# Kernel tuning notes

Hardware: AMD Instinct MI355X
Metric: run time of the kernel (lower is better)

Reference implementation:

```python
import jax, jax.numpy as jnp
from jax import lax
import numpy as np

STRIDE = 1
PADDING = 1
THRESHOLD = 0.25
DECAY = 0.9


def setup_inputs() -> dict:
    key = jax.random.key(0)
    k1, k2 = jax.random.split(key)
    B, Cin, L, T = 16, 32, 1024, 64
    Cout, K = 64, 3
    x = jax.random.uniform(k1, (B, Cin, L, T), dtype=jnp.float32)
    weight = jax.random.normal(k2, (Cout, Cin, K), dtype=jnp.float32) * 0.1
    return {"x": x, "weight": weight}


def reference(x, weight):
    # x: (B, Cin, L, T); weight: (Cout, Cin, K)
    B, Cin, L, T = x.shape
    Cout, _, K = weight.shape
    # Conv1d applied to every timestep at once: fold T into the batch dim.
    xt = jnp.transpose(x, (0, 3, 1, 2)).reshape(B * T, Cin, L)  # (B*T, Cin, L)
    act = lax.conv_general_dilated(
        xt, weight,
        window_strides=(STRIDE,),
        padding=[(PADDING, PADDING)],
        dimension_numbers=("NCH", "OIH", "NCH"),
    )  # (B*T, Cout, OL)
    OL = act.shape[-1]
    act = act.reshape(B, T, Cout, OL).transpose(1, 0, 2, 3)  # (T, B, Cout, OL)

    def step(pot, a):
        # LIF update: integrate, decay, threshold, reset (matches original order).
        pot = (pot + a) * DECAY
        spk = (pot >= THRESHOLD).astype(pot.dtype)
        pot = jnp.where(spk > 0, jnp.zeros_like(pot), pot)
        return pot, spk

    pot0 = jnp.zeros((B, Cout, OL), dtype=x.dtype)
    _, spikes = lax.scan(step, pot0, act)  # spikes: (T, B, Cout, OL)
    return jnp.transpose(spikes, (1, 2, 3, 0))  # (B, Cout, OL, T)
```

## Files before the change

### kernel.cpp

```cpp
#include <hip/hip_runtime.h>
#include <math.h>

#define BB    16
#define CIN   32
#define LEN   1024
#define TT    64
#define COUT  64
#define KK    3

#define TL      32
#define HALO    (TL + 2)
#define TCH     8
#define PADT    12
#define CO_PER  8
#define NTHREADS 256
#define NROWS   (CIN * HALO)
#define NITEM   (NROWS * 2)
#define NPRE    ((NITEM + NTHREADS - 1) / NTHREADS)


__device__ __forceinline__ float4 load_item(const float* __restrict__ xb,
                                            int l0, int tc, int idx) {
    const int row = idx >> 1;
    const int h   = idx & 1;
    const int ci  = row / HALO;
    const int ll  = row % HALO;
    const int lg  = l0 - 1 + ll;
    float4 v = make_float4(0.f, 0.f, 0.f, 0.f);
    if (lg >= 0 && lg < LEN)
        v = *(const float4*)(xb + ((size_t)ci * LEN + lg) * TT + tc * TCH + h * 4);
    return v;
}

__global__ __launch_bounds__(NTHREADS)
void snn_v3(const float* __restrict__ x, const float* __restrict__ w,
            float* __restrict__ out) {
    __shared__ float xs[CIN][HALO][PADT];

    const int tid  = threadIdx.x;
    const int l    = tid & 31;
    const int half = (tid >> 5) & 1;
    const int wvu  = __builtin_amdgcn_readfirstlane(tid >> 6);
    const int coA  = wvu * 16;
    const int l0   = blockIdx.x * TL;
    const int b    = blockIdx.y;

    const float* xb   = x   + (size_t)b * CIN * LEN * TT;
    float*       outb = out + (size_t)b * COUT * LEN * TT;

    float pot[CO_PER];
    #pragma unroll
    for (int j = 0; j < CO_PER; ++j) pot[j] = 0.0f;

    float4 pre[NPRE];
    {
        int i = 0;
        for (int idx = tid; idx < NITEM; idx += NTHREADS, ++i)
            pre[i] = load_item(xb, l0, 0, idx);
    }

    for (int tc = 0; tc < TT / TCH; ++tc) {
        __syncthreads();
        {
            int i = 0;
            for (int idx = tid; idx < NITEM; idx += NTHREADS, ++i) {
                const int row = idx >> 1;
                const int h   = idx & 1;
                *(float4*)&xs[row / HALO][row % HALO][h * 4] = pre[i];
            }
        }
        __syncthreads();
        if (tc + 1 < TT / TCH) {
            int i = 0;
            for (int idx = tid; idx < NITEM; idx += NTHREADS, ++i)
                pre[i] = load_item(xb, l0, tc + 1, idx);
        }

        float acc[CO_PER][TCH];
        #pragma unroll
        for (int j = 0; j < CO_PER; ++j)
            #pragma unroll
            for (int i = 0; i < TCH; ++i) acc[j][i] = 0.0f;

        #pragma unroll
        for (int k = 0; k < KK; ++k) {
            for (int ci = 0; ci < CIN; ++ci) {
                const float4 xa = *(const float4*)&xs[ci][l + k][0];
                const float4 xc = *(const float4*)&xs[ci][l + k][4];
                #pragma unroll
                for (int j = 0; j < CO_PER; ++j) {
                    const float wA = w[((coA + j)     * CIN + ci) * KK + k];
                    const float wB = w[((coA + 8 + j) * CIN + ci) * KK + k];
                    const float wj = half ? wB : wA;
                    acc[j][0] = fmaf(xa.x, wj, acc[j][0]);
                    acc[j][1] = fmaf(xa.y, wj, acc[j][1]);
                    acc[j][2] = fmaf(xa.z, wj, acc[j][2]);
                    acc[j][3] = fmaf(xa.w, wj, acc[j][3]);
                    acc[j][4] = fmaf(xc.x, wj, acc[j][4]);
                    acc[j][5] = fmaf(xc.y, wj, acc[j][5]);
                    acc[j][6] = fmaf(xc.z, wj, acc[j][6]);
                    acc[j][7] = fmaf(xc.w, wj, acc[j][7]);
                }
            }
        }

        const int co0 = coA + half * 8;
        #pragma unroll
        for (int j = 0; j < CO_PER; ++j) {
            float sv[TCH];
            #pragma unroll
            for (int i = 0; i < TCH; ++i) {
                const float s = pot[j] + acc[j][i];
                const float p = s * 0.9f;
                const bool spk = (p >= 0.25f);
                sv[i]  = spk ? 1.0f : 0.0f;
                pot[j] = spk ? 0.0f : p;
            }
            float* dst = outb + ((size_t)(co0 + j) * LEN + (l0 + l)) * TT
                              + tc * TCH;
            *(float4*)(dst)     = make_float4(sv[0], sv[1], sv[2], sv[3]);
            *(float4*)(dst + 4) = make_float4(sv[4], sv[5], sv[6], sv[7]);
        }
    }
}

extern "C" void kernel_launch(void* const* d_in, const int* in_sizes, int n_in,
                              void* d_out, int out_size, void* d_ws, size_t ws_size,
                              hipStream_t stream) {
    const float* x = (const float*)d_in[0];
    const float* w = (const float*)d_in[1];
    float* out = (float*)d_out;
    (void)d_ws; (void)ws_size; (void)in_sizes; (void)n_in; (void)out_size;

    hipLaunchKernelGGL(snn_v3, dim3(LEN / TL, BB), dim3(NTHREADS),
                       0, stream, x, w, out);
}
```

Baseline: 722.6 us.

## Restructure SNN conv kernel with smaller tiles, swizzled LDS and bit-packed spikes

Shrinks the L tile to 16 positions and gives each thread 4 output channels instead of 8. The time axis is staged in 16-wide chunks through an XOR-swizzled float4 shared buffer. Spikes are collected into bitmasks in registers and written once at the end as contiguous 64-float rows per output channel, replacing the strided per-chunk writes. The aim is higher occupancy (launch bounds 4), fewer LDS bank conflicts and more coalesced stores. In exchange the grid has twice as many blocks with more halo reloads, and the software prefetch across chunks is gone.

```diff
diff --git a/kernel.cpp b/kernel.cpp
--- a/kernel.cpp
+++ b/kernel.cpp
@@ -1,5 +1,4 @@
 #include <hip/hip_runtime.h>
-#include <math.h>
 
 #define BB    16
 #define CIN   32
@@ -8,118 +7,140 @@
 #define COUT  64
 #define KK    3
 
-#define TL      32
-#define HALO    (TL + 2)
-#define TCH     8
-#define PADT    12
-#define CO_PER  8
+#define TL       16
+#define HALO     (TL + 2)
 #define NTHREADS 256
-#define NROWS   (CIN * HALO)
-#define NITEM   (NROWS * 2)
-#define NPRE    ((NITEM + NTHREADS - 1) / NTHREADS)
+#define CO_PER   4
+#define NGRAN    (CIN * HALO * 4)
+#define NRND     (NGRAN / 64)
+#define SPT      (NRND / 4)
 
 
-__device__ __forceinline__ float4 load_item(const float* __restrict__ xb,
-                                            int l0, int tc, int idx) {
-    const int row = idx >> 1;
-    const int h   = idx & 1;
-    const int ci  = row / HALO;
-    const int ll  = row % HALO;
-    const int lg  = l0 - 1 + ll;
-    float4 v = make_float4(0.f, 0.f, 0.f, 0.f);
-    if (lg >= 0 && lg < LEN)
-        v = *(const float4*)(xb + ((size_t)ci * LEN + lg) * TT + tc * TCH + h * 4);
-    return v;
-}
-
-__global__ __launch_bounds__(NTHREADS)
-void snn_v3(const float* __restrict__ x, const float* __restrict__ w,
+__global__ __launch_bounds__(NTHREADS, 4)
+void snn_v4(const float* __restrict__ x, const float* __restrict__ w,
             float* __restrict__ out) {
-    __shared__ float xs[CIN][HALO][PADT];
+    __shared__ float4 xs[NGRAN];
 
     const int tid  = threadIdx.x;
-    const int l    = tid & 31;
-    const int half = (tid >> 5) & 1;
-    const int wvu  = __builtin_amdgcn_readfirstlane(tid >> 6);
-    const int coA  = wvu * 16;
+    const int l    = tid & (TL - 1);
+    const int g    = tid >> 4;
+    const int co0  = g * CO_PER;
+    const int lane = tid & 63;
+    const int wv   = tid >> 6;
     const int l0   = blockIdx.x * TL;
     const int b    = blockIdx.y;
 
-    const float* xb   = x   + (size_t)b * CIN * LEN * TT;
-    float*       outb = out + (size_t)b * COUT * LEN * TT;
+    const float* xb = x + (size_t)b * CIN * LEN * TT;
+    const float* wb = w + co0 * (CIN * KK);
 
-    float pot[CO_PER];
+    int goff[SPT], loff[SPT];
+    unsigned okb = 0u;
     #pragma unroll
-    for (int j = 0; j < CO_PER; ++j) pot[j] = 0.0f;
-
-    float4 pre[NPRE];
-    {
-        int i = 0;
-        for (int idx = tid; idx < NITEM; idx += NTHREADS, ++i)
-            pre[i] = load_item(xb, l0, 0, idx);
+    for (int s = 0; s < SPT; ++s) {
+        const int G   = (wv + s * 4) * 64 + lane;
+        const int ci  = G / (HALO * 4);
+        const int rem = G - ci * (HALO * 4);
+        const int row = rem >> 2;
+        const int h   = rem & 3;
+        const int lg  = l0 - 1 + row;
+        const bool ok = (lg >= 0) && (lg < LEN);
+        okb |= ok ? (1u << s) : 0u;
+        goff[s] = (ci * LEN + (ok ? lg : 0)) * TT + h * 4;
+        loff[s] = ci * (HALO * 4) + row * 4 + (h ^ ((row >> 1) & 3));
     }
 
-    for (int tc = 0; tc < TT / TCH; ++tc) {
-        __syncthreads();
-        {
-            int i = 0;
-            for (int idx = tid; idx < NITEM; idx += NTHREADS, ++i) {
-                const int row = idx >> 1;
-                const int h   = idx & 1;
-                *(float4*)&xs[row / HALO][row % HALO][h * 4] = pre[i];
-            }
+    float    pot[CO_PER] = {0.f, 0.f, 0.f, 0.f};
+    unsigned mlo[CO_PER] = {0u, 0u, 0u, 0u};
+    unsigned mhi[CO_PER] = {0u, 0u, 0u, 0u};
+    float4   tmp[SPT];
+
+    auto issue_loads = [&](int sc) {
+        #pragma unroll
+        for (int s = 0; s < SPT; ++s) {
+            tmp[s] = make_float4(0.f, 0.f, 0.f, 0.f);
+            if (okb & (1u << s))
+                tmp[s] = *(const float4*)(xb + goff[s] + sc * 16);
         }
-        __syncthreads();
-        if (tc + 1 < TT / TCH) {
-            int i = 0;
-            for (int idx = tid; idx < NITEM; idx += NTHREADS, ++i)
-                pre[i] = load_item(xb, l0, tc + 1, idx);
-        }
+    };
 
-        float acc[CO_PER][TCH];
+    auto substage = [&](int sub, int sc) {
+        float acc[CO_PER][8];
         #pragma unroll
         for (int j = 0; j < CO_PER; ++j)
             #pragma unroll
-            for (int i = 0; i < TCH; ++i) acc[j][i] = 0.0f;
+            for (int i = 0; i < 8; ++i) acc[j][i] = 0.f;
 
         #pragma unroll
         for (int k = 0; k < KK; ++k) {
-            for (int ci = 0; ci < CIN; ++ci) {
-                const float4 xa = *(const float4*)&xs[ci][l + k][0];
-                const float4 xc = *(const float4*)&xs[ci][l + k][4];
+            const int rowk = l + k;
+            const int sw   = (rowk >> 1) & 3;
+            const int sA   = rowk * 4 + ((sub * 2)     ^ sw);
+            const int sB   = rowk * 4 + ((sub * 2 + 1) ^ sw);
+            #pragma unroll 1
+            for (int cic = 0; cic < CIN / 4; ++cic) {
                 #pragma unroll
-                for (int j = 0; j < CO_PER; ++j) {
-                    const float wA = w[((coA + j)     * CIN + ci) * KK + k];
-                    const float wB = w[((coA + 8 + j) * CIN + ci) * KK + k];
-                    const float wj = half ? wB : wA;
-                    acc[j][0] = fmaf(xa.x, wj, acc[j][0]);
-                    acc[j][1] = fmaf(xa.y, wj, acc[j][1]);
-                    acc[j][2] = fmaf(xa.z, wj, acc[j][2]);
-                    acc[j][3] = fmaf(xa.w, wj, acc[j][3]);
-                    acc[j][4] = fmaf(xc.x, wj, acc[j][4]);
-                    acc[j][5] = fmaf(xc.y, wj, acc[j][5]);
-                    acc[j][6] = fmaf(xc.z, wj, acc[j][6]);
-                    acc[j][7] = fmaf(xc.w, wj, acc[j][7]);
+                for (int c4 = 0; c4 < 4; ++c4) {
+                    const int ci = cic * 4 + c4;
+                    const float4 xa = xs[ci * (HALO * 4) + sA];
+                    const float4 xc = xs[ci * (HALO * 4) + sB];
+                    #pragma unroll
+                    for (int j = 0; j < CO_PER; ++j) {
+                        const float wj = wb[j * (CIN * KK) + ci * KK + k];
+                        acc[j][0] = fmaf(xa.x, wj, acc[j][0]);
+                        acc[j][1] = fmaf(xa.y, wj, acc[j][1]);
+                        acc[j][2] = fmaf(xa.z, wj, acc[j][2]);
+                        acc[j][3] = fmaf(xa.w, wj, acc[j][3]);
+                        acc[j][4] = fmaf(xc.x, wj, acc[j][4]);
+                        acc[j][5] = fmaf(xc.y, wj, acc[j][5]);
+                        acc[j][6] = fmaf(xc.z, wj, acc[j][6]);
+                        acc[j][7] = fmaf(xc.w, wj, acc[j][7]);
+                    }
                 }
             }
         }
 
-        const int co0 = coA + half * 8;
         #pragma unroll
         for (int j = 0; j < CO_PER; ++j) {
-            float sv[TCH];
+            unsigned sb = 0u;
             #pragma unroll
-            for (int i = 0; i < TCH; ++i) {
-                const float s = pot[j] + acc[j][i];
-                const float p = s * 0.9f;
-                const bool spk = (p >= 0.25f);
-                sv[i]  = spk ? 1.0f : 0.0f;
-                pot[j] = spk ? 0.0f : p;
+            for (int i = 0; i < 8; ++i) {
+                const float s  = pot[j] + acc[j][i];
+                const float p  = s * 0.9f;
+                const bool  sp = (p >= 0.25f);
+                sb |= sp ? (1u << i) : 0u;
+                pot[j] = sp ? 0.0f : p;
             }
-            float* dst = outb + ((size_t)(co0 + j) * LEN + (l0 + l)) * TT
-                              + tc * TCH;
-            *(float4*)(dst)     = make_float4(sv[0], sv[1], sv[2], sv[3]);
-            *(float4*)(dst + 4) = make_float4(sv[4], sv[5], sv[6], sv[7]);
+            const unsigned sh = (unsigned)((sc & 1) * 16 + sub * 8);
+            if (sc < 2) mlo[j] |= sb << sh;
+            else        mhi[j] |= sb << sh;
+        }
+    };
+
+    #pragma unroll 1
+    for (int sc = 0; sc < 4; ++sc) {
+        issue_loads(sc);
+        __syncthreads();
+        #pragma unroll
+        for (int s = 0; s < SPT; ++s) xs[loff[s]] = tmp[s];
+        __syncthreads();
+        substage(0, sc);
+        substage(1, sc);
+    }
+
+    float* outb = out + (size_t)b * COUT * LEN * TT;
+    #pragma unroll
+    for (int j = 0; j < CO_PER; ++j) {
+        float* dst = outb + ((size_t)(co0 + j) * LEN + (l0 + l)) * TT;
+        #pragma unroll
+        for (int tq = 0; tq < 16; ++tq) {
+            const unsigned word = (tq < 8) ? mlo[j] : mhi[j];
+            const unsigned nib  = word >> ((tq & 7) * 4);
+            float4 v;
+            v.x = (nib & 1u) ? 1.0f : 0.0f;
+            v.y = (nib & 2u) ? 1.0f : 0.0f;
+            v.z = (nib & 4u) ? 1.0f : 0.0f;
+            v.w = (nib & 8u) ? 1.0f : 0.0f;
+            *(float4*)(dst + tq * 4) = v;
         }
     }
 }
@@ -132,6 +153,6 @@
     float* out = (float*)d_out;
     (void)d_ws; (void)ws_size; (void)in_sizes; (void)n_in; (void)out_size;
 
-    hipLaunchKernelGGL(snn_v3, dim3(LEN / TL, BB), dim3(NTHREADS),
+    hipLaunchKernelGGL(snn_v4, dim3(LEN / TL, BB), dim3(NTHREADS),
                        0, stream, x, w, out);
 }
```

Result: faster. 624.4 us (-13.6%).

## Rewrite conv+LIF kernel with time-split waves, async LDS loads, and repacked weights

Applied to the files above, without the earlier changes.

Replaces the time-chunked loop with a single-pass kernel. Each block loads the full 64-timestep halo tile for 8 positions straight into swizzled LDS using global_load_lds. Each wave computes 16 timesteps for 8 output channels, and the LIF scan is carried across the four waves in sequence by passing the potential through LDS. Weights are repacked into a contiguous per-group layout by a separate pre-kernel, and the block index is remapped for locality. This removes the register prefetch staging and the per-chunk barriers, at the cost of a serialized LIF tail, an extra kernel launch, and higher register pressure.

```diff
diff --git a/kernel.cpp b/kernel.cpp
--- a/kernel.cpp
+++ b/kernel.cpp
@@ -1,5 +1,4 @@
 #include <hip/hip_runtime.h>
-#include <math.h>
 
 #define BB    16
 #define CIN   32
@@ -8,120 +7,185 @@
 #define COUT  64
 #define KK    3
 
-#define TL      32
-#define HALO    (TL + 2)
-#define TCH     8
-#define PADT    12
-#define CO_PER  8
+#define TL       8
+#define HALO     10
 #define NTHREADS 256
-#define NROWS   (CIN * HALO)
-#define NITEM   (NROWS * 2)
-#define NPRE    ((NITEM + NTHREADS - 1) / NTHREADS)
-
-
-__device__ __forceinline__ float4 load_item(const float* __restrict__ xb,
-                                            int l0, int tc, int idx) {
-    const int row = idx >> 1;
-    const int h   = idx & 1;
-    const int ci  = row / HALO;
-    const int ll  = row % HALO;
-    const int lg  = l0 - 1 + ll;
-    float4 v = make_float4(0.f, 0.f, 0.f, 0.f);
-    if (lg >= 0 && lg < LEN)
-        v = *(const float4*)(xb + ((size_t)ci * LEN + lg) * TT + tc * TCH + h * 4);
-    return v;
+#define NGRAN    (CIN * HALO * 16)
+#define NROUND   (NGRAN / 64)
+#define RPW      (NROUND / 4)
+
+
+__device__ float wpk8[COUT * CIN * KK];
+__device__ float zeros_g[64];
+
+__global__ void repack_w(const float* __restrict__ w) {
+    const int i = blockIdx.x * 256 + threadIdx.x;
+    if (i < COUT * CIN * KK) {
+        const int j  = i & 7;
+        const int ci = (i >> 3) & 31;
+        const int gk = i >> 8;
+        const int k  = gk % 3;
+        const int g  = gk / 3;
+        wpk8[i] = w[((g * 8 + j) * CIN + ci) * KK + k];
+    }
 }
 
-__global__ __launch_bounds__(NTHREADS)
-void snn_v3(const float* __restrict__ x, const float* __restrict__ w,
-            float* __restrict__ out) {
-    __shared__ float xs[CIN][HALO][PADT];
+#define GLD16(GP, LP) __builtin_amdgcn_global_load_lds(                      \
+    (const __attribute__((address_space(1))) void*)(GP),                     \
+    (__attribute__((address_space(3))) void*)(LP), 16, 0, 0)
+
+__global__ __launch_bounds__(NTHREADS, 2)
+void snn_v7(const float* __restrict__ x, float* __restrict__ out) {
+    __shared__ float4 xs[NGRAN];
 
     const int tid  = threadIdx.x;
-    const int l    = tid & 31;
-    const int half = (tid >> 5) & 1;
-    const int wvu  = __builtin_amdgcn_readfirstlane(tid >> 6);
-    const int coA  = wvu * 16;
-    const int l0   = blockIdx.x * TL;
-    const int b    = blockIdx.y;
+    const int l    = tid & 7;
+    const int g    = (tid >> 3) & 7;
+    const int lane = tid & 63;
+    const int tq2  = __builtin_amdgcn_readfirstlane(tid >> 6);
+
+    const int lin = blockIdx.x;
+    const int wid = (lin & 7) * 256 + (lin >> 3);
+    const int b   = wid >> 7;
+    const int lx  = wid & 127;
+    const int l0  = lx * TL;
+    const int lo  = l0 + l;
 
     const float* xb   = x   + (size_t)b * CIN * LEN * TT;
     float*       outb = out + (size_t)b * COUT * LEN * TT;
 
-    float pot[CO_PER];
+    int off[RPW];
+    unsigned okm = 0u;
     #pragma unroll
-    for (int j = 0; j < CO_PER; ++j) pot[j] = 0.0f;
-
-    float4 pre[NPRE];
+    for (int m = 0; m < RPW; ++m) {
+        const int G   = (tq2 * RPW + m) * 64 + lane;
+        const int ci  = G / (HALO * 16);
+        const int rem = G - ci * (HALO * 16);
+        const int row = rem >> 4;
+        const int gp  = rem & 15;
+        const int tqs = gp ^ (row & 7);
+        const int lg  = l0 - 1 + row;
+        const bool ok = (lg >= 0) && (lg < LEN);
+        okm |= ok ? (1u << m) : 0u;
+        off[m] = (ci * LEN + (ok ? lg : 0)) * TT + tqs * 4;
+    }
     {
-        int i = 0;
-        for (int idx = tid; idx < NITEM; idx += NTHREADS, ++i)
-            pre[i] = load_item(xb, l0, 0, idx);
-    }
-
-    for (int tc = 0; tc < TT / TCH; ++tc) {
-        __syncthreads();
-        {
-            int i = 0;
-            for (int idx = tid; idx < NITEM; idx += NTHREADS, ++i) {
-                const int row = idx >> 1;
-                const int h   = idx & 1;
-                *(float4*)&xs[row / HALO][row % HALO][h * 4] = pre[i];
-            }
-        }
-        __syncthreads();
-        if (tc + 1 < TT / TCH) {
-            int i = 0;
-            for (int idx = tid; idx < NITEM; idx += NTHREADS, ++i)
-                pre[i] = load_item(xb, l0, tc + 1, idx);
-        }
-
-        float acc[CO_PER][TCH];
+        char* lb = (char*)xs + tq2 * (RPW * 1024);
         #pragma unroll
-        for (int j = 0; j < CO_PER; ++j)
+        for (int m = 0; m < RPW; ++m) {
+            const float* sp = (okm & (1u << m)) ? (xb + off[m]) : zeros_g;
+            GLD16(sp, lb + m * 1024);
+        }
+    }
+    __syncthreads();
+
+    float acc[8][16];
+    #pragma unroll
+    for (int j = 0; j < 8; ++j)
+        #pragma unroll
+        for (int t = 0; t < 16; ++t) acc[j][t] = 0.f;
+
+    const float* wq  = wpk8 + g * (KK * CIN * 8);
+    const char*  xsb = (const char*)xs;
+
+    #pragma unroll
+    for (int k = 0; k < KK; ++k) {
+        const int row = l + k;
+        const int r7  = row & 7;
+        const int rb  = row * 256;
+        const char* a0 = xsb + rb + ((((tq2 * 4 + 0) ^ r7)) << 4);
+        const char* a1 = xsb + rb + ((((tq2 * 4 + 1) ^ r7)) << 4);
+        const char* a2 = xsb + rb + ((((tq2 * 4 + 2) ^ r7)) << 4);
+        const char* a3 = xsb + rb + ((((tq2 * 4 + 3) ^ r7)) << 4);
+        #pragma unroll 1
+        for (int cic = 0; cic < 4; ++cic) {
+            const float* wqa = wq + k * (CIN * 8) + cic * 64;
             #pragma unroll
-            for (int i = 0; i < TCH; ++i) acc[j][i] = 0.0f;
-
-        #pragma unroll
-        for (int k = 0; k < KK; ++k) {
-            for (int ci = 0; ci < CIN; ++ci) {
-                const float4 xa = *(const float4*)&xs[ci][l + k][0];
-                const float4 xc = *(const float4*)&xs[ci][l + k][4];
+            for (int c8 = 0; c8 < 8; ++c8) {
+                const float4 x0 = *(const float4*)(a0 + c8 * 2560);
+                const float4 x1 = *(const float4*)(a1 + c8 * 2560);
+                const float4 x2 = *(const float4*)(a2 + c8 * 2560);
+                const float4 x3 = *(const float4*)(a3 + c8 * 2560);
+                const float4 wa = *(const float4*)(wqa + c8 * 8);
+                const float4 wb = *(const float4*)(wqa + c8 * 8 + 4);
                 #pragma unroll
-                for (int j = 0; j < CO_PER; ++j) {
-                    const float wA = w[((coA + j)     * CIN + ci) * KK + k];
-                    const float wB = w[((coA + 8 + j) * CIN + ci) * KK + k];
-                    const float wj = half ? wB : wA;
-                    acc[j][0] = fmaf(xa.x, wj, acc[j][0]);
-                    acc[j][1] = fmaf(xa.y, wj, acc[j][1]);
-                    acc[j][2] = fmaf(xa.z, wj, acc[j][2]);
-                    acc[j][3] = fmaf(xa.w, wj, acc[j][3]);
-                    acc[j][4] = fmaf(xc.x, wj, acc[j][4]);
-                    acc[j][5] = fmaf(xc.y, wj, acc[j][5]);
-                    acc[j][6] = fmaf(xc.z, wj, acc[j][6]);
-                    acc[j][7] = fmaf(xc.w, wj, acc[j][7]);
+                for (int j = 0; j < 8; ++j) {
+                    const float w = (j == 0) ? wa.x : (j == 1) ? wa.y
+                                  : (j == 2) ? wa.z : (j == 3) ? wa.w
+                                  : (j == 4) ? wb.x : (j == 5) ? wb.y
+                                  : (j == 6) ? wb.z : wb.w;
+                    acc[j][ 0] = fmaf(x0.x, w, acc[j][ 0]);
+                    acc[j][ 1] = fmaf(x0.y, w, acc[j][ 1]);
+                    acc[j][ 2] = fmaf(x0.z, w, acc[j][ 2]);
+                    acc[j][ 3] = fmaf(x0.w, w, acc[j][ 3]);
+                    acc[j][ 4] = fmaf(x1.x, w, acc[j][ 4]);
+                    acc[j][ 5] = fmaf(x1.y, w, acc[j][ 5]);
+                    acc[j][ 6] = fmaf(x1.z, w, acc[j][ 6]);
+                    acc[j][ 7] = fmaf(x1.w, w, acc[j][ 7]);
+                    acc[j][ 8] = fmaf(x2.x, w, acc[j][ 8]);
+                    acc[j][ 9] = fmaf(x2.y, w, acc[j][ 9]);
+                    acc[j][10] = fmaf(x2.z, w, acc[j][10]);
+                    acc[j][11] = fmaf(x2.w, w, acc[j][11]);
+                    acc[j][12] = fmaf(x3.x, w, acc[j][12]);
+                    acc[j][13] = fmaf(x3.y, w, acc[j][13]);
+                    acc[j][14] = fmaf(x3.z, w, acc[j][14]);
+                    acc[j][15] = fmaf(x3.w, w, acc[j][15]);
                 }
             }
-        }
-
-        const int co0 = coA + half * 8;
-        #pragma unroll
-        for (int j = 0; j < CO_PER; ++j) {
-            float sv[TCH];
-            #pragma unroll
-            for (int i = 0; i < TCH; ++i) {
-                const float s = pot[j] + acc[j][i];
-                const float p = s * 0.9f;
-                const bool spk = (p >= 0.25f);
-                sv[i]  = spk ? 1.0f : 0.0f;
-                pot[j] = spk ? 0.0f : p;
-            }
-            float* dst = outb + ((size_t)(co0 + j) * LEN + (l0 + l)) * TT
-                              + tc * TCH;
-            *(float4*)(dst)     = make_float4(sv[0], sv[1], sv[2], sv[3]);
-            *(float4*)(dst + 4) = make_float4(sv[4], sv[5], sv[6], sv[7]);
-        }
-    }
+            a0 += 8 * 2560; a1 += 8 * 2560; a2 += 8 * 2560; a3 += 8 * 2560;
+        }
+    }
+
+    __syncthreads();
+    float* potb = (float*)xs;
+
+    float    pp[8];
+    unsigned bits[8];
+
+    #define LIF_SCAN(FIRST)                                                  \
+        {   _Pragma("unroll")                                                \
+            for (int j = 0; j < 8; ++j) {                                    \
+                float p = (FIRST) ? 0.f : potb[lane * 8 + j];                \
+                unsigned sb = 0u;                                            \
+                _Pragma("unroll")                                            \
+                for (int t = 0; t < 16; ++t) {                               \
+                    const float s  = p + acc[j][t];                          \
+                    const float q  = s * 0.9f;                               \
+                    const bool  sp = (q >= 0.25f);                           \
+                    sb |= sp ? (1u << t) : 0u;                               \
+                    p = sp ? 0.f : q;                                        \
+                }                                                            \
+                pp[j] = p; bits[j] = sb;                                     \
+            }                                                                \
+        }
+    #define POT_WRITE()                                                      \
+        {   _Pragma("unroll")                                                \
+            for (int j = 0; j < 8; ++j) potb[lane * 8 + j] = pp[j];          \
+        }
+    #define STORE_Q()                                                        \
+        {   _Pragma("unroll")                                                \
+            for (int j = 0; j < 8; ++j) {                                    \
+                float* dst = outb + ((size_t)(g * 8 + j) * LEN + lo) * TT    \
+                                  + tq2 * 16;                                \
+                _Pragma("unroll")                                            \
+                for (int q4 = 0; q4 < 4; ++q4) {                             \
+                    const unsigned nib = bits[j] >> (q4 * 4);                \
+                    *(float4*)(dst + q4 * 4) =                               \
+                        make_float4(nib & 1u ? 1.f : 0.f,                    \
+                                    nib & 2u ? 1.f : 0.f,                    \
+                                    nib & 4u ? 1.f : 0.f,                    \
+                                    nib & 8u ? 1.f : 0.f);                   \
+                }                                                            \
+            }                                                                \
+        }
+
+    if (tq2 == 0) { LIF_SCAN(true);  POT_WRITE(); STORE_Q(); }
+    __syncthreads();
+    if (tq2 == 1) { LIF_SCAN(false); POT_WRITE(); STORE_Q(); }
+    __syncthreads();
+    if (tq2 == 2) { LIF_SCAN(false); POT_WRITE(); STORE_Q(); }
+    __syncthreads();
+    if (tq2 == 3) { LIF_SCAN(false);              STORE_Q(); }
 }
 
 extern "C" void kernel_launch(void* const* d_in, const int* in_sizes, int n_in,
@@ -132,6 +196,7 @@
     float* out = (float*)d_out;
     (void)d_ws; (void)ws_size; (void)in_sizes; (void)n_in; (void)out_size;
 
-    hipLaunchKernelGGL(snn_v3, dim3(LEN / TL, BB), dim3(NTHREADS),
-                       0, stream, x, w, out);
+    hipLaunchKernelGGL(repack_w, dim3(24), dim3(256), 0, stream, w);
+    hipLaunchKernelGGL(snn_v7, dim3((LEN / TL) * BB), dim3(NTHREADS),
+                       0, stream, x, out);
 }
```

After: 723.5 us. No clear change (+0.1%).
